# Kernel optimization log

Hardware: AMD Instinct MI355X
Metric: run time of the kernel (lower is better)

Reference implementation:

```python
import jax, jax.numpy as jnp
import numpy as np

B, N, D, H = 4, 1024, 1024, 16
DH = D // H
EPS = 1e-5


def setup_inputs() -> dict:
    key = jax.random.key(0)
    ks = jax.random.split(key, 16)
    s = lambda fan_in: 1.0 / np.sqrt(fan_in)
    inp = {
        'x0': jax.random.normal(ks[0], (B, N, D), jnp.float32),
        'x1': jax.random.normal(ks[1], (B, N, D), jnp.float32),
        # weights stored as [in, out]; y = x @ W + b
        'Wqk': jax.random.uniform(ks[2], (D, D), jnp.float32, -s(D), s(D)),
        'bqk': jax.random.uniform(ks[3], (D,), jnp.float32, -s(D), s(D)),
        'Wv': jax.random.uniform(ks[4], (D, D), jnp.float32, -s(D), s(D)),
        'bv': jax.random.uniform(ks[5], (D,), jnp.float32, -s(D), s(D)),
        'Wo': jax.random.uniform(ks[6], (D, D), jnp.float32, -s(D), s(D)),
        'bo': jax.random.uniform(ks[7], (D,), jnp.float32, -s(D), s(D)),
        'Wf1': jax.random.uniform(ks[8], (2 * D, 2 * D), jnp.float32, -s(2 * D), s(2 * D)),
        'bf1': jax.random.uniform(ks[9], (2 * D,), jnp.float32, -s(2 * D), s(2 * D)),
        'gamma': jnp.ones((2 * D,), jnp.float32),
        'beta': jnp.zeros((2 * D,), jnp.float32),
        'Wf2': jax.random.uniform(ks[10], (2 * D, D), jnp.float32, -s(2 * D), s(2 * D)),
        'bf2': jax.random.uniform(ks[11], (D,), jnp.float32, -s(2 * D), s(2 * D)),
    }
    return inp


def _heads(t):
    # [B, N, D] -> [B, H, N, DH]
    b, n, _ = t.shape
    return t.reshape(b, n, H, DH).transpose(0, 2, 1, 3)


def _merge(t):
    # [B, H, N, DH] -> [B, N, D]
    b, h, n, dh = t.shape
    return t.transpose(0, 2, 1, 3).reshape(b, n, h * dh)


def _ffn(z, Wf1, bf1, gamma, beta, Wf2, bf2):
    h = z @ Wf1 + bf1
    mu = jnp.mean(h, axis=-1, keepdims=True)
    var = jnp.mean((h - mu) ** 2, axis=-1, keepdims=True)
    h = (h - mu) * jax.lax.rsqrt(var + EPS) * gamma + beta
    h = jax.nn.gelu(h, approximate=False)
    return h @ Wf2 + bf2


def reference(x0, x1, Wqk, bqk, Wv, bv, Wo, bo, Wf1, bf1, gamma, beta, Wf2, bf2):
    scale = DH ** (-0.5)
    qk0 = _heads(x0 @ Wqk + bqk) * (scale ** 0.5)
    qk1 = _heads(x1 @ Wqk + bqk) * (scale ** 0.5)
    v0 = _heads(x0 @ Wv + bv)
    v1 = _heads(x1 @ Wv + bv)
    # shared similarity matrix [B, H, N0, N1]
    sim = jnp.einsum('bhid,bhjd->bhij', qk0, qk1)
    attn01 = jax.nn.softmax(sim, axis=-1)            # over N1
    attn10 = jax.nn.softmax(sim, axis=-2)            # over N0 (== softmax(sim^T, -1)^T)
    m0 = jnp.einsum('bhij,bhjd->bhid', attn01, v1)   # [B,H,N0,DH]
    m1 = jnp.einsum('bhji,bhjd->bhid', attn10, v0)   # [B,H,N1,DH]
    m0 = _merge(m0) @ Wo + bo
    m1 = _merge(m1) @ Wo + bo
    y0 = x0 + _ffn(jnp.concatenate([x0, m0], -1), Wf1, bf1, gamma, beta, Wf2, bf2)
    y1 = x1 + _ffn(jnp.concatenate([x1, m1], -1), Wf1, bf1, gamma, beta, Wf2, bf2)
    return (y0, y1)
```

## Files before the change

### kernel.cpp

```cpp
#include <hip/hip_runtime.h>
#include <hip/hip_bf16.h>

typedef unsigned short u16;
typedef unsigned int u32;
typedef __attribute__((ext_vector_type(8))) short bf16x8;
typedef __attribute__((ext_vector_type(4))) float f32x4;
typedef __attribute__((ext_vector_type(16))) float f32x16;

#define DEV __device__ __forceinline__
#define FENCE asm volatile("" ::: "memory")
#define WAITL asm volatile("s_waitcnt lgkmcnt(0)" ::: "memory")
#define BAR __builtin_amdgcn_s_barrier()
#define VMC(n) asm volatile("s_waitcnt vmcnt(" #n ")" ::: "memory")

static constexpr int Bc = 4, Nc = 1024, Dc = 1024, Hc = 16, Mc = 4096, D2c = 2048;
static constexpr size_t VT_STRIDE = (size_t)4 * 16 * 64 * 1024;

DEV u16 f2bf(float f) {
  u32 u = __builtin_bit_cast(u32, f);
  u = (u + 0x7FFFu + ((u >> 16) & 1u)) >> 16;
  return (u16)u;
}
DEV float bf2f(u16 h) { u32 u = ((u32)h) << 16; return __builtin_bit_cast(float, u); }
DEV void gl_lds16(const void* g, void* l) {
  __builtin_amdgcn_global_load_lds((const __attribute__((address_space(1))) u32*)g,
                                   (__attribute__((address_space(3))) u32*)l, 16, 0, 0);
}
DEV int SW(int r, int c) { return c ^ (r & 7) ^ ((r >> 3) & 3); }

DEV float erf_fast(float x) {
  float ax = __builtin_fabsf(x);
  float t = __builtin_amdgcn_rcpf(__builtin_fmaf(0.3275911f, ax, 1.0f));
  float p = __builtin_fmaf(1.061405429f, t, -1.453152027f);
  p = __builtin_fmaf(p, t, 1.421413741f);
  p = __builtin_fmaf(p, t, -0.284496736f);
  p = __builtin_fmaf(p, t, 0.254829592f);
  p *= t;
  float e = __builtin_amdgcn_exp2f(-1.4426950408889634f * ax * ax);
  float r = __builtin_fmaf(-p, e, 1.0f);
  return __builtin_copysignf(r, x);
}
DEV float gelu_exact(float v) {
  return 0.5f * v * (1.0f + erf_fast(v * 0.70710678118654752f));
}

__global__ __launch_bounds__(256) void k_f32_to_bf16(const float* __restrict__ in,
                                                     u16* __restrict__ out, int n) {
  int i = (blockIdx.x * 256 + threadIdx.x) * 8;
  if (i >= n) return;
  float4 a = *(const float4*)(in + i);
  float4 b = *(const float4*)(in + i + 4);
  union { u16 s[8]; uint4 v; } r;
  r.s[0] = f2bf(a.x); r.s[1] = f2bf(a.y); r.s[2] = f2bf(a.z); r.s[3] = f2bf(a.w);
  r.s[4] = f2bf(b.x); r.s[5] = f2bf(b.y); r.s[6] = f2bf(b.z); r.s[7] = f2bf(b.w);
  *(uint4*)(out + i) = r.v;
}

__global__ __launch_bounds__(256) void k_transpose_f32_bf16(const float* __restrict__ in,
                                                            u16* __restrict__ out, int R, int C) {
  __shared__ float t[64][65];
  int c0 = blockIdx.x * 64, r0 = blockIdx.y * 64;
  int tid = threadIdx.x;
  int rr = tid >> 4, cc4 = (tid & 15) * 4;
  for (int k = 0; k < 4; ++k) {
    int r = rr + k * 16;
    float4 v = *(const float4*)(in + (size_t)(r0 + r) * C + c0 + cc4);
    t[r][cc4 + 0] = v.x; t[r][cc4 + 1] = v.y; t[r][cc4 + 2] = v.z; t[r][cc4 + 3] = v.w;
  }
  __syncthreads();
  int cw = tid >> 4, rr4 = (tid & 15) * 4;
  for (int k = 0; k < 4; ++k) {
    int c = cw + k * 16;
    union { u16 s[4]; uint2 v; } p;
    for (int j = 0; j < 4; ++j) p.s[j] = f2bf(t[rr4 + j][c]);
    *(uint2*)(out + (size_t)(c0 + c) * R + r0 + rr4) = p.v;
  }
}

__global__ __launch_bounds__(256) void k_v_transpose(const u16* __restrict__ qkv,
                                                     u16* __restrict__ vt01) {
  __shared__ __align__(16) u16 t[64][80];
  int z = blockIdx.z;
  const u16* v = qkv + (size_t)z * Mc * 2048 + 1024;
  u16* vt = vt01 + (size_t)z * VT_STRIDE;
  int nt = blockIdx.x;
  int bh = blockIdx.y, b = bh >> 4, h = bh & 15;
  int tid = threadIdx.x;
  for (int it = 0; it < 2; ++it) {
    int u = it * 256 + tid; int r = u >> 3, ch = u & 7;
    uint4 raw = *(const uint4*)(v + ((size_t)b * Nc + nt * 64 + r) * 2048 + h * 64 + ch * 8);
    *(uint4*)&t[r][ch * 8] = raw;
  }
  __syncthreads();
  for (int it = 0; it < 2; ++it) {
    int u = it * 256 + tid; int d = u >> 3, nch = u & 7;
    union { u16 s[8]; uint4 v4; } p;
    for (int j = 0; j < 8; ++j) p.s[j] = t[nch * 8 + j][d];
    *(uint4*)(vt + ((size_t)bh * 64 + d) * Nc + nt * 64 + nch * 8) = p.v4;
  }
}

__global__ __launch_bounds__(512, 1) void k_gemm8(
    const u16* __restrict__ A1, int lda1, const u16* __restrict__ A2, int lda2, int kstile,
    const u16* __restrict__ Bt, const float* __restrict__ bias1, const float* __restrict__ bias2,
    int Nsplit, float scale1, float scale2, u16* __restrict__ out, int ldc, int K, int gx) {
  __shared__ __align__(16) u16 lds[65536];
  int tid = threadIdx.x;
  int w = tid >> 6, l = tid & 63;
  int lo = l & 15, hi = l >> 4;
  int wm2 = w >> 2, wn4 = w & 3;
  int nt = K >> 6, niter = nt >> 1;

  int nwg = gridDim.x;
  int swz = (blockIdx.x & 7) * (nwg >> 3) + (blockIdx.x >> 3);
  int m0 = (swz / gx) * 256, n0 = (swz % gx) * 256;

  auto ldsA = [&](int buf, int h) -> u16* { return lds + ((buf << 1) + h) * 8192; };
  auto ldsB = [&](int buf, int h) -> u16* { return lds + 32768 + ((buf << 1) + h) * 8192; };

  auto stageA = [&](int tile, int h) {
    int tt = tile < nt ? tile : 0;
    const u16* base; int ldx, kof;
    if (tt < kstile) { base = A1; ldx = lda1; kof = tt * 64; }
    else             { base = A2; ldx = lda2; kof = (tt - kstile) * 64; }
    u16* dst = ldsA(tile & 1, h);
    size_t row0 = (size_t)(m0 + h * 128);
#pragma unroll
    for (int i = 0; i < 2; ++i) {
      int e = i * 4096 + tid * 8;
      int r = e >> 6, s = (e >> 3) & 7;
      gl_lds16(base + (row0 + r) * (size_t)ldx + kof + 8 * (s ^ (r & 7)), dst + e);
    }
  };
  auto stageB = [&](int tile, int h) {
    int tt = tile < nt ? tile : 0;
    u16* dst = ldsB(tile & 1, h);
    size_t row0 = (size_t)(n0 + h * 128);
#pragma unroll
    for (int i = 0; i < 2; ++i) {
      int e = i * 4096 + tid * 8;
      int r = e >> 6, s = (e >> 3) & 7;
      gl_lds16(Bt + (row0 + r) * (size_t)K + tt * 64 + 8 * (s ^ (r & 7)), dst + e);
    }
  };
  auto loadA = [&](bf16x8 (&a)[4][2], int buf, int qm) {
    const u16* src = ldsA(buf, qm);
#pragma unroll
    for (int mf = 0; mf < 4; ++mf) {
      int r = wm2 * 64 + mf * 16 + lo;
#pragma unroll
      for (int kk = 0; kk < 2; ++kk)
        a[mf][kk] = *(const bf16x8*)&src[r * 64 + (((kk * 4 + hi) ^ (r & 7)) << 3)];
    }
  };
  auto loadB = [&](bf16x8 (&bq)[2][2], int buf, int qn) {
    const u16* src = ldsB(buf, qn);
#pragma unroll
    for (int nf = 0; nf < 2; ++nf) {
      int r = wn4 * 32 + nf * 16 + lo;
#pragma unroll
      for (int kk = 0; kk < 2; ++kk)
        bq[nf][kk] = *(const bf16x8*)&src[r * 64 + (((kk * 4 + hi) ^ (r & 7)) << 3)];
    }
  };

  f32x4 acc00[4][2] = {}, acc01[4][2] = {}, acc10[4][2] = {}, acc11[4][2] = {};
  bf16x8 a[4][2], b0[2][2], b1[2][2];

  auto mmaQ = [&](f32x4 (&accq)[4][2], bf16x8 (&aa)[4][2], bf16x8 (&bb)[2][2]) {
    __builtin_amdgcn_s_setprio(1);
#pragma unroll
    for (int mf = 0; mf < 4; ++mf)
#pragma unroll
      for (int nf = 0; nf < 2; ++nf)
#pragma unroll
        for (int kk = 0; kk < 2; ++kk)
          accq[mf][nf] = __builtin_amdgcn_mfma_f32_16x16x32_bf16(aa[mf][kk], bb[nf][kk], accq[mf][nf], 0, 0, 0);
    __builtin_amdgcn_s_setprio(0);
  };

  stageA(0, 0); stageB(0, 0); stageB(0, 1); stageA(0, 1);
  stageA(1, 0); stageB(1, 0); stageB(1, 1); stageA(1, 1);
  VMC(12); BAR;

  for (int it = 0; it < niter; ++it) {
    int t0 = 2 * it;
    loadA(a, 0, 0); loadB(b0, 0, 0);
    FENCE; BAR; WAITL;
    mmaQ(acc00, a, b0);
    FENCE; VMC(10); BAR;
    loadB(b1, 0, 1);
    stageA(t0 + 2, 0);
    FENCE; BAR; WAITL;
    mmaQ(acc01, a, b1);
    FENCE; VMC(10); BAR;
    loadA(a, 0, 1);
    stageB(t0 + 2, 0);
    FENCE; BAR; WAITL;
    mmaQ(acc10, a, b0);
    FENCE; BAR;
    stageB(t0 + 2, 1);
    FENCE; BAR;
    mmaQ(acc11, a, b1);
    FENCE; VMC(10); BAR;
    loadA(a, 1, 0); loadB(b0, 1, 0);
    stageA(t0 + 2, 1);
    FENCE; BAR; WAITL;
    mmaQ(acc00, a, b0);
    FENCE; VMC(10); BAR;
    loadB(b1, 1, 1);
    stageA(t0 + 3, 0);
    FENCE; BAR; WAITL;
    mmaQ(acc01, a, b1);
    FENCE; VMC(10); BAR;
    loadA(a, 1, 1);
    stageB(t0 + 3, 0);
    FENCE; BAR; WAITL;
    mmaQ(acc10, a, b0);
    FENCE; BAR;
    stageB(t0 + 3, 1); stageA(t0 + 3, 1);
    FENCE; BAR;
    mmaQ(acc11, a, b1);
    FENCE; VMC(12); BAR;
  }

  auto epi = [&](f32x4 (&accq)[4][2], int qm, int qn) {
#pragma unroll
    for (int mf = 0; mf < 4; ++mf)
#pragma unroll
      for (int nf = 0; nf < 2; ++nf) {
        int col = n0 + qn * 128 + wn4 * 32 + nf * 16 + lo;
        float bb, sc;
        if (col < Nsplit) { bb = bias1[col]; sc = scale1; }
        else              { bb = bias2[col - Nsplit]; sc = scale2; }
        int row = m0 + qm * 128 + wm2 * 64 + mf * 16 + hi * 4;
#pragma unroll
        for (int i = 0; i < 4; ++i)
          out[(size_t)(row + i) * ldc + col] = f2bf((accq[mf][nf][i] + bb) * sc);
      }
  };
  epi(acc00, 0, 0); epi(acc01, 0, 1); epi(acc10, 1, 0); epi(acc11, 1, 1);
}

template <bool OUT_BF16>
__global__ __launch_bounds__(512, 1) void k_gemm8h(
    const u16* __restrict__ A1, int lda1, const u16* __restrict__ Bt,
    const float* __restrict__ bias,
    const float* __restrict__ resid0, const float* __restrict__ resid1, int Msplit,
    void* __restrict__ out, int ldc, int K, int gx) {
  __shared__ __align__(16) u16 lds[49152];
  int tid = threadIdx.x;
  int w = tid >> 6, l = tid & 63;
  int lo = l & 15, hi = l >> 4;
  int wm2 = w >> 2, wn4 = w & 3;
  int nt = K >> 6, niter = nt >> 1;

  int nwg = gridDim.x;
  int swz = (blockIdx.x & 7) * (nwg >> 3) + (blockIdx.x >> 3);
  int m0 = (swz / gx) * 256, n0 = (swz % gx) * 128;

  auto ldsA = [&](int buf, int h) -> u16* { return lds + ((buf << 1) + h) * 8192; };
  auto ldsB = [&](int buf, int h) -> u16* { return lds + 32768 + ((buf << 1) + h) * 4096; };

  auto stageA = [&](int tile, int h) {
    int tt = tile < nt ? tile : 0;
    u16* dst = ldsA(tile & 1, h);
    size_t row0 = (size_t)(m0 + h * 128);
#pragma unroll
    for (int i = 0; i < 2; ++i) {
      int e = i * 4096 + tid * 8;
      int r = e >> 6, s = (e >> 3) & 7;
      gl_lds16(A1 + (row0 + r) * (size_t)lda1 + tt * 64 + 8 * (s ^ (r & 7)), dst + e);
    }
  };
  auto stageB = [&](int tile, int h) {
    int tt = tile < nt ? tile : 0;
    u16* dst = ldsB(tile & 1, h);
    size_t row0 = (size_t)(n0 + h * 64);
    int e = tid * 8;
    int r = e >> 6, s = (e >> 3) & 7;
    gl_lds16(Bt + (row0 + r) * (size_t)K + tt * 64 + 8 * (s ^ (r & 7)), dst + e);
  };
  auto loadA = [&](bf16x8 (&a)[4][2], int buf, int qm) {
    const u16* src = ldsA(buf, qm);
#pragma unroll
    for (int mf = 0; mf < 4; ++mf) {
      int r = wm2 * 64 + mf * 16 + lo;
#pragma unroll
      for (int kk = 0; kk < 2; ++kk)
        a[mf][kk] = *(const bf16x8*)&src[r * 64 + (((kk * 4 + hi) ^ (r & 7)) << 3)];
    }
  };
  auto loadB = [&](bf16x8 (&bq)[2], int buf, int qn) {
    const u16* src = ldsB(buf, qn);
    int r = wn4 * 16 + lo;
#pragma unroll
    for (int kk = 0; kk < 2; ++kk)
      bq[kk] = *(const bf16x8*)&src[r * 64 + (((kk * 4 + hi) ^ (r & 7)) << 3)];
  };

  f32x4 acc00[4] = {}, acc01[4] = {}, acc10[4] = {}, acc11[4] = {};
  bf16x8 a[4][2], b0[2], b1[2];

  auto mma8 = [&](f32x4 (&accq)[4], bf16x8 (&aa)[4][2], bf16x8 (&bb)[2]) {
    __builtin_amdgcn_s_setprio(1);
#pragma unroll
    for (int mf = 0; mf < 4; ++mf)
#pragma unroll
      for (int kk = 0; kk < 2; ++kk)
        accq[mf] = __builtin_amdgcn_mfma_f32_16x16x32_bf16(aa[mf][kk], bb[kk], accq[mf], 0, 0, 0);
    __builtin_amdgcn_s_setprio(0);
  };

  stageA(0, 0); stageB(0, 0); stageB(0, 1); stageA(0, 1);
  stageA(1, 0); stageB(1, 0); stageB(1, 1); stageA(1, 1);
  VMC(9); BAR;

  for (int it = 0; it < niter; ++it) {
    int t0 = 2 * it;
    loadA(a, 0, 0); loadB(b0, 0, 0);
    FENCE; BAR; WAITL;
    mma8(acc00, a, b0);
    FENCE; VMC(8); BAR;
    loadB(b1, 0, 1);
    stageA(t0 + 2, 0);
    FENCE; BAR; WAITL;
    mma8(acc01, a, b1);
    FENCE; VMC(8); BAR;
    loadA(a, 0, 1);
    stageB(t0 + 2, 0);
    FENCE; BAR; WAITL;
    mma8(acc10, a, b0);
    FENCE; BAR;
    stageB(t0 + 2, 1);
    FENCE; BAR;
    mma8(acc11, a, b1);
    FENCE; VMC(7); BAR;
    loadA(a, 1, 0); loadB(b0, 1, 0);
    stageA(t0 + 2, 1);
    FENCE; BAR; WAITL;
    mma8(acc00, a, b0);
    FENCE; VMC(8); BAR;
    loadB(b1, 1, 1);
    stageA(t0 + 3, 0);
    FENCE; BAR; WAITL;
    mma8(acc01, a, b1);
    FENCE; VMC(8); BAR;
    loadA(a, 1, 1);
    stageB(t0 + 3, 0);
    FENCE; BAR; WAITL;
    mma8(acc10, a, b0);
    FENCE; BAR;
    stageB(t0 + 3, 1); stageA(t0 + 3, 1);
    FENCE; BAR;
    mma8(acc11, a, b1);
    FENCE; VMC(9); BAR;
  }

  auto epi = [&](f32x4 (&accq)[4], int qm, int qn) {
    int col = n0 + qn * 64 + wn4 * 16 + lo;
    float bb = bias[col];
#pragma unroll
    for (int mf = 0; mf < 4; ++mf) {
      int row = m0 + qm * 128 + wm2 * 64 + mf * 16 + hi * 4;
      const float* rsd = nullptr; int roff = 0;
      if (resid0) { if (row < Msplit) { rsd = resid0; } else { rsd = resid1; roff = Msplit; } }
#pragma unroll
      for (int i = 0; i < 4; ++i) {
        float v = accq[mf][i] + bb;
        if (rsd) v += rsd[(size_t)(row + i - roff) * ldc + col];
        if (OUT_BF16) ((u16*)out)[(size_t)(row + i) * ldc + col] = f2bf(v);
        else          ((float*)out)[(size_t)(row + i) * ldc + col] = v;
      }
    }
  };
  epi(acc00, 0, 0); epi(acc01, 0, 1); epi(acc10, 1, 0); epi(acc11, 1, 1);
}

__global__ __launch_bounds__(512, 2) void k_attn(const u16* __restrict__ qkv,
                                                 const u16* __restrict__ vt01,
                                                 u16* __restrict__ m01) {
  __shared__ __align__(16) u16 q_lds[256 * 64];
  __shared__ __align__(16) u16 k_lds[2][64 * 64];
  __shared__ __align__(16) u16 v_lds[2][64 * 64];
  int z = blockIdx.z;
  const u16* Q  = qkv + (size_t)z * Mc * 2048;
  const u16* Kg = qkv + (size_t)(1 - z) * Mc * 2048;
  const u16* Vt = vt01 + (size_t)(1 - z) * VT_STRIDE;
  u16* Out = m01 + (size_t)z * Mc * Dc;
  int tid = threadIdx.x;
  int w = tid >> 6, l = tid & 63;
  int q31 = l & 31, h = l >> 5;
  int qt = blockIdx.x;
  int bh = blockIdx.y, b = bh >> 4, hd = bh & 15;
  size_t rowQ0 = (size_t)b * Nc + qt * 256;

  {
    int r = tid >> 3, s = tid & 7;
#pragma unroll
    for (int c = 0; c < 4; ++c)
      gl_lds16(Q + (rowQ0 + c * 64 + r) * 2048 + hd * 64 + 8 * SW(r, s),
               &q_lds[(size_t)(c * 512 + tid) * 8]);
    gl_lds16(Kg + ((size_t)b * Nc + r) * 2048 + hd * 64 + 8 * SW(r, s), &k_lds[0][(size_t)tid * 8]);
    gl_lds16(Vt + ((size_t)bh * 64 + r) * Nc + 8 * SW(r, s), &v_lds[0][(size_t)tid * 8]);
  }
  __syncthreads();

  bf16x8 qf[4];
  {
    int row = w * 32 + q31;
#pragma unroll
    for (int dk = 0; dk < 4; ++dk)
      qf[dk] = *(const bf16x8*)&q_lds[row * 64 + (SW(row, dk * 2 + h) << 3)];
  }

  f32x16 o0 = {}, o1 = {};
  float ls = 0.f;
  int cur = 0;

  for (int t = 0; t < Nc / 64; ++t) {
    if (t + 1 < Nc / 64) {
      int r = tid >> 3, s = tid & 7;
      gl_lds16(Kg + ((size_t)b * Nc + (t + 1) * 64 + r) * 2048 + hd * 64 + 8 * SW(r, s),
               &k_lds[cur ^ 1][(size_t)tid * 8]);
      gl_lds16(Vt + ((size_t)bh * 64 + r) * Nc + (t + 1) * 64 + 8 * SW(r, s),
               &v_lds[cur ^ 1][(size_t)tid * 8]);
    }

    f32x16 s0 = {}, s1 = {};
    __builtin_amdgcn_s_setprio(1);
#pragma unroll
    for (int dk = 0; dk < 4; ++dk) {
      int r0 = q31, r1 = 32 + q31;
      bf16x8 k0 = *(const bf16x8*)&k_lds[cur][r0 * 64 + (SW(r0, dk * 2 + h) << 3)];
      bf16x8 k1 = *(const bf16x8*)&k_lds[cur][r1 * 64 + (SW(r1, dk * 2 + h) << 3)];
      s0 = __builtin_amdgcn_mfma_f32_32x32x16_bf16(k0, qf[dk], s0, 0, 0, 0);
      s1 = __builtin_amdgcn_mfma_f32_32x32x16_bf16(k1, qf[dk], s1, 0, 0, 0);
    }
    __builtin_amdgcn_s_setprio(0);

    {
      float c16[16];
#pragma unroll
      for (int i = 0; i < 16; ++i) {
        float p0 = exp2f(s0[i]);
        float p1 = exp2f(s1[i]);
        s0[i] = p0; s1[i] = p1;
        c16[i] = p0 + p1;
      }
#pragma unroll
      for (int st = 8; st >= 1; st >>= 1)
#pragma unroll
        for (int i = 0; i < st; ++i) c16[i] += c16[i + st];
      u32 xa = __builtin_bit_cast(u32, c16[0]), xb = xa;
      asm("v_permlane32_swap_b32 %0, %1" : "+v"(xa), "+v"(xb));
      ls += __builtin_bit_cast(float, xa) + __builtin_bit_cast(float, xb);
    }

    u32 pk0[4][2], pk1[4][2];
#pragma unroll
    for (int a2 = 0; a2 < 4; ++a2)
#pragma unroll
      for (int c2 = 0; c2 < 2; ++c2) {
        asm("v_cvt_pk_bf16_f32 %0, %1, %2" : "=v"(pk0[a2][c2]) : "v"(s0[4 * a2 + 2 * c2]), "v"(s0[4 * a2 + 2 * c2 + 1]));
        asm("v_cvt_pk_bf16_f32 %0, %1, %2" : "=v"(pk1[a2][c2]) : "v"(s1[4 * a2 + 2 * c2]), "v"(s1[4 * a2 + 2 * c2 + 1]));
      }
    bf16x8 pf[4];
#pragma unroll
    for (int ks = 0; ks < 4; ++ks) {
      const int aE = (2 * ks) & 3, aO = (2 * ks + 1) & 3;
      u32 x0, y0, x1, y1;
      if (ks < 2) { x0 = pk0[aE][0]; y0 = pk0[aO][0]; x1 = pk0[aE][1]; y1 = pk0[aO][1]; }
      else        { x0 = pk1[aE][0]; y0 = pk1[aO][0]; x1 = pk1[aE][1]; y1 = pk1[aO][1]; }
      asm("v_permlane32_swap_b32 %0, %1" : "+v"(x0), "+v"(y0));
      asm("v_permlane32_swap_b32 %0, %1" : "+v"(x1), "+v"(y1));
      union { u32 u[4]; bf16x8 v; } fu;
      fu.u[0] = x0; fu.u[1] = x1; fu.u[2] = y0; fu.u[3] = y1;
      pf[ks] = fu.v;
    }

    __builtin_amdgcn_s_setprio(1);
#pragma unroll
    for (int ks = 0; ks < 4; ++ks) {
      int r0 = q31, r1 = 32 + q31;
      bf16x8 v0 = *(const bf16x8*)&v_lds[cur][r0 * 64 + (SW(r0, ks * 2 + h) << 3)];
      bf16x8 v1 = *(const bf16x8*)&v_lds[cur][r1 * 64 + (SW(r1, ks * 2 + h) << 3)];
      o0 = __builtin_amdgcn_mfma_f32_32x32x16_bf16(v0, pf[ks], o0, 0, 0, 0);
      o1 = __builtin_amdgcn_mfma_f32_32x32x16_bf16(v1, pf[ks], o1, 0, 0, 0);
    }
    __builtin_amdgcn_s_setprio(0);

    __syncthreads();
    cur ^= 1;
  }

  float inv = 1.f / ls;
  int q_abs = qt * 256 + w * 32 + q31;
  u16* orow = Out + ((size_t)b * Nc + q_abs) * Dc + hd * 64;
#pragma unroll
  for (int rq = 0; rq < 4; ++rq) {
    union { u16 s[4]; uint2 v; } p0, p1;
#pragma unroll
    for (int c = 0; c < 4; ++c) {
      p0.s[c] = f2bf(o0[4 * rq + c] * inv);
      p1.s[c] = f2bf(o1[4 * rq + c] * inv);
    }
    *(uint2*)(orow + 8 * rq + 4 * h) = p0.v;
    *(uint2*)(orow + 32 + 8 * rq + 4 * h) = p1.v;
  }
}

__global__ __launch_bounds__(256) void k_ln_gelu(u16* __restrict__ hbuf,
                                                 const float* __restrict__ gamma,
                                                 const float* __restrict__ beta) {
  int w = threadIdx.x >> 6, l = threadIdx.x & 63;
  int row = blockIdx.x * 4 + w;
  u16* hp = hbuf + (size_t)row * D2c;

  uint4 raw[4];
#pragma unroll
  for (int i = 0; i < 4; ++i)
    raw[i] = *(const uint4*)(hp + (i * 64 + l) * 8);

  float vals[32];
  float s = 0.f, s2 = 0.f;
#pragma unroll
  for (int i = 0; i < 4; ++i) {
    const u16* rs = (const u16*)&raw[i];
#pragma unroll
    for (int j = 0; j < 8; ++j) {
      float v = bf2f(rs[j]);
      vals[i * 8 + j] = v;
      s += v; s2 += v * v;
    }
  }
#pragma unroll
  for (int off = 1; off < 64; off <<= 1) {
    s += __shfl_xor(s, off);
    s2 += __shfl_xor(s2, off);
  }
  float mu = s * (1.f / D2c);
  float var = s2 * (1.f / D2c) - mu * mu;
  float rstd = rsqrtf(var + 1e-5f);

#pragma unroll
  for (int i = 0; i < 4; ++i) {
    int cbase = (i * 64 + l) * 8;
    float4 g0 = *(const float4*)(gamma + cbase);
    float4 g1 = *(const float4*)(gamma + cbase + 4);
    float4 b0 = *(const float4*)(beta + cbase);
    float4 b1 = *(const float4*)(beta + cbase + 4);
    float g[8] = {g0.x, g0.y, g0.z, g0.w, g1.x, g1.y, g1.z, g1.w};
    float bt[8] = {b0.x, b0.y, b0.z, b0.w, b1.x, b1.y, b1.z, b1.w};
    union { u16 s[8]; uint4 v; } o;
#pragma unroll
    for (int j = 0; j < 8; ++j) {
      float v = (vals[i * 8 + j] - mu) * rstd * g[j] + bt[j];
      o.s[j] = f2bf(gelu_exact(v));
    }
    *(uint4*)(hp + cbase) = o.v;
  }
}

extern "C" void kernel_launch(void* const* d_in, const int* in_sizes, int n_in,
                              void* d_out, int out_size, void* d_ws, size_t ws_size,
                              hipStream_t stream) {
  const float* x0   = (const float*)d_in[0];
  const float* x1   = (const float*)d_in[1];
  const float* Wqk  = (const float*)d_in[2];
  const float* bqk  = (const float*)d_in[3];
  const float* Wv   = (const float*)d_in[4];
  const float* bv   = (const float*)d_in[5];
  const float* Wo   = (const float*)d_in[6];
  const float* bo   = (const float*)d_in[7];
  const float* Wf1  = (const float*)d_in[8];
  const float* bf1  = (const float*)d_in[9];
  const float* gamma= (const float*)d_in[10];
  const float* beta = (const float*)d_in[11];
  const float* Wf2  = (const float*)d_in[12];
  const float* bf2  = (const float*)d_in[13];
  float* y = (float*)d_out;

  char* p = (char*)d_ws;
  auto take = [&](size_t elems) { u16* r = (u16*)p; p += ((elems * 2 + 255) & ~(size_t)255); return r; };
  u16* Wqkvt = take((size_t)2048 * 1024);
  u16* Wot   = take((size_t)1024 * 1024);
  u16* Wf1t  = take((size_t)2048 * 2048);
  u16* Wf2t  = take((size_t)2048 * 1024);
  u16* x01b  = take((size_t)8192 * 1024);
  u16* qkv   = take((size_t)8192 * 2048);
  u16* vt01  = take(2 * VT_STRIDE);
  u16* m01   = take((size_t)8192 * 1024);
  u16* h01 = qkv;
  u16* o01 = vt01;

  dim3 blk(256);
  const float sq = 0.4246608984f;

  k_transpose_f32_bf16<<<dim3(16, 16), blk, 0, stream>>>(Wqk, Wqkvt, 1024, 1024);
  k_transpose_f32_bf16<<<dim3(16, 16), blk, 0, stream>>>(Wv, Wqkvt + (size_t)1024 * 1024, 1024, 1024);
  k_transpose_f32_bf16<<<dim3(16, 16), blk, 0, stream>>>(Wo, Wot, 1024, 1024);
  k_transpose_f32_bf16<<<dim3(32, 32), blk, 0, stream>>>(Wf1, Wf1t, 2048, 2048);
  k_transpose_f32_bf16<<<dim3(16, 32), blk, 0, stream>>>(Wf2, Wf2t, 2048, 1024);
  k_f32_to_bf16<<<dim3(2048), blk, 0, stream>>>(x0, x01b, 4096 * 1024);
  k_f32_to_bf16<<<dim3(2048), blk, 0, stream>>>(x1, x01b + (size_t)4096 * 1024, 4096 * 1024);

  k_gemm8<<<dim3(256), dim3(512), 0, stream>>>(
      x01b, 1024, x01b, 1024, 16, Wqkvt,
      bqk, bv, 1024, sq, 1.f, qkv, 2048, 1024, 8);

  k_v_transpose<<<dim3(16, 64, 2), blk, 0, stream>>>(qkv, vt01);

  k_attn<<<dim3(4, 64, 2), dim3(512), 0, stream>>>(qkv, vt01, m01);

  k_gemm8h<true><<<dim3(256), dim3(512), 0, stream>>>(
      m01, 1024, Wot, bo, nullptr, nullptr, 0, o01, 1024, 1024, 8);

  k_gemm8<<<dim3(256), dim3(512), 0, stream>>>(
      x01b, 1024, o01, 1024, 16, Wf1t,
      bf1, nullptr, 2048, 1.f, 1.f, h01, 2048, 2048, 8);

  k_ln_gelu<<<dim3(2048), blk, 0, stream>>>(h01, gamma, beta);

  k_gemm8h<false><<<dim3(256), dim3(512), 0, stream>>>(
      h01, 2048, Wf2t, bf2, x0, x1, 4096, y, 1024, 2048, 8);
}
```

Measured before the change: 285.2 us.

## Double-buffer A fragments and overlap LDS reads with MFMA in GEMM main loops

```diff
diff --git a/kernel.cpp b/kernel.cpp
--- a/kernel.cpp
+++ b/kernel.cpp
@@ -9,9 +9,10 @@
 
 #define DEV __device__ __forceinline__
 #define FENCE asm volatile("" ::: "memory")
-#define WAITL asm volatile("s_waitcnt lgkmcnt(0)" ::: "memory")
 #define BAR __builtin_amdgcn_s_barrier()
 #define VMC(n) asm volatile("s_waitcnt vmcnt(" #n ")" ::: "memory")
+#define LGKM(n) asm volatile("s_waitcnt lgkmcnt(" #n ")" ::: "memory")
+#define SGB __builtin_amdgcn_sched_barrier(0)
 
 static constexpr int Bc = 4, Nc = 1024, Dc = 1024, Hc = 16, Mc = 4096, D2c = 2048;
 static constexpr size_t VT_STRIDE = (size_t)4 * 16 * 64 * 1024;
@@ -165,63 +166,68 @@
   };
 
   f32x4 acc00[4][2] = {}, acc01[4][2] = {}, acc10[4][2] = {}, acc11[4][2] = {};
-  bf16x8 a[4][2], b0[2][2], b1[2][2];
+  bf16x8 a_A[4][2], a_B[4][2], b0[2][2], b1[2][2];
 
   auto mmaQ = [&](f32x4 (&accq)[4][2], bf16x8 (&aa)[4][2], bf16x8 (&bb)[2][2]) {
     __builtin_amdgcn_s_setprio(1);
 #pragma unroll
-    for (int mf = 0; mf < 4; ++mf)
-#pragma unroll
-      for (int nf = 0; nf < 2; ++nf)
-#pragma unroll
-        for (int kk = 0; kk < 2; ++kk)
+    for (int kk = 0; kk < 2; ++kk)
+#pragma unroll
+      for (int mf = 0; mf < 4; ++mf)
+#pragma unroll
+        for (int nf = 0; nf < 2; ++nf)
           accq[mf][nf] = __builtin_amdgcn_mfma_f32_16x16x32_bf16(aa[mf][kk], bb[nf][kk], accq[mf][nf], 0, 0, 0);
     __builtin_amdgcn_s_setprio(0);
   };
 
   stageA(0, 0); stageB(0, 0); stageB(0, 1); stageA(0, 1);
   stageA(1, 0); stageB(1, 0); stageB(1, 1); stageA(1, 1);
-  VMC(12); BAR;
+  VMC(10); BAR;
+  loadA(a_A, 0, 0);
+  loadB(b0, 0, 0);
+  FENCE;
 
   for (int it = 0; it < niter; ++it) {
     int t0 = 2 * it;
-    loadA(a, 0, 0); loadB(b0, 0, 0);
-    FENCE; BAR; WAITL;
-    mmaQ(acc00, a, b0);
-    FENCE; VMC(10); BAR;
     loadB(b1, 0, 1);
+    LGKM(4); SGB;
+    mmaQ(acc00, a_A, b0);
+    VMC(8); BAR;
+    loadA(a_B, 0, 1);
     stageA(t0 + 2, 0);
-    FENCE; BAR; WAITL;
-    mmaQ(acc01, a, b1);
-    FENCE; VMC(10); BAR;
-    loadA(a, 0, 1);
+    LGKM(8); SGB;
+    mmaQ(acc01, a_A, b1);
+    BAR;
     stageB(t0 + 2, 0);
-    FENCE; BAR; WAITL;
-    mmaQ(acc10, a, b0);
-    FENCE; BAR;
+    LGKM(0); SGB;
+    mmaQ(acc11, a_B, b1);
+    VMC(8); BAR;
+    loadA(a_A, 1, 0);
     stageB(t0 + 2, 1);
-    FENCE; BAR;
-    mmaQ(acc11, a, b1);
-    FENCE; VMC(10); BAR;
-    loadA(a, 1, 0); loadB(b0, 1, 0);
+    SGB;
+    mmaQ(acc10, a_B, b0);
+    loadB(b0, 1, 0);
+    VMC(6); BAR;
+    loadB(b1, 1, 1);
     stageA(t0 + 2, 1);
-    FENCE; BAR; WAITL;
-    mmaQ(acc00, a, b0);
-    FENCE; VMC(10); BAR;
-    loadB(b1, 1, 1);
+    LGKM(4); SGB;
+    mmaQ(acc00, a_A, b0);
+    BAR;
+    loadA(a_B, 1, 1);
     stageA(t0 + 3, 0);
-    FENCE; BAR; WAITL;
-    mmaQ(acc01, a, b1);
-    FENCE; VMC(10); BAR;
-    loadA(a, 1, 1);
+    LGKM(8); SGB;
+    mmaQ(acc01, a_A, b1);
+    BAR;
     stageB(t0 + 3, 0);
-    FENCE; BAR; WAITL;
-    mmaQ(acc10, a, b0);
-    FENCE; BAR;
+    LGKM(0); SGB;
+    mmaQ(acc11, a_B, b1);
+    VMC(8); BAR;
+    loadA(a_A, 0, 0);
     stageB(t0 + 3, 1); stageA(t0 + 3, 1);
-    FENCE; BAR;
-    mmaQ(acc11, a, b1);
-    FENCE; VMC(12); BAR;
+    SGB;
+    mmaQ(acc10, a_B, b0);
+    loadB(b0, 0, 0);
+    VMC(10); BAR;
   }
 
   auto epi = [&](f32x4 (&accq)[4][2], int qm, int qn) {
@@ -239,7 +245,7 @@
           out[(size_t)(row + i) * ldc + col] = f2bf((accq[mf][nf][i] + bb) * sc);
       }
   };
-  epi(acc00, 0, 0); epi(acc01, 0, 1); epi(acc10, 1, 0); epi(acc11, 1, 1);
+  epi(acc00, 0, 0); epi(acc01, 0, 1); epi(acc11, 1, 1); epi(acc10, 1, 0);
 }
 
 template <bool OUT_BF16>
@@ -300,61 +306,66 @@
   };
 
   f32x4 acc00[4] = {}, acc01[4] = {}, acc10[4] = {}, acc11[4] = {};
-  bf16x8 a[4][2], b0[2], b1[2];
+  bf16x8 a_A[4][2], a_B[4][2], b0[2], b1[2];
 
   auto mma8 = [&](f32x4 (&accq)[4], bf16x8 (&aa)[4][2], bf16x8 (&bb)[2]) {
     __builtin_amdgcn_s_setprio(1);
 #pragma unroll
-    for (int mf = 0; mf < 4; ++mf)
-#pragma unroll
-      for (int kk = 0; kk < 2; ++kk)
+    for (int kk = 0; kk < 2; ++kk)
+#pragma unroll
+      for (int mf = 0; mf < 4; ++mf)
         accq[mf] = __builtin_amdgcn_mfma_f32_16x16x32_bf16(aa[mf][kk], bb[kk], accq[mf], 0, 0, 0);
     __builtin_amdgcn_s_setprio(0);
   };
 
   stageA(0, 0); stageB(0, 0); stageB(0, 1); stageA(0, 1);
   stageA(1, 0); stageB(1, 0); stageB(1, 1); stageA(1, 1);
-  VMC(9); BAR;
+  VMC(8); BAR;
+  loadA(a_A, 0, 0);
+  loadB(b0, 0, 0);
+  FENCE;
 
   for (int it = 0; it < niter; ++it) {
     int t0 = 2 * it;
-    loadA(a, 0, 0); loadB(b0, 0, 0);
-    FENCE; BAR; WAITL;
-    mma8(acc00, a, b0);
-    FENCE; VMC(8); BAR;
     loadB(b1, 0, 1);
+    LGKM(2); SGB;
+    mma8(acc00, a_A, b0);
+    VMC(6); BAR;
+    loadA(a_B, 0, 1);
     stageA(t0 + 2, 0);
-    FENCE; BAR; WAITL;
-    mma8(acc01, a, b1);
-    FENCE; VMC(8); BAR;
-    loadA(a, 0, 1);
+    LGKM(8); SGB;
+    mma8(acc01, a_A, b1);
+    BAR;
     stageB(t0 + 2, 0);
-    FENCE; BAR; WAITL;
-    mma8(acc10, a, b0);
-    FENCE; BAR;
+    LGKM(0); SGB;
+    mma8(acc11, a_B, b1);
+    VMC(6); BAR;
+    loadA(a_A, 1, 0);
     stageB(t0 + 2, 1);
-    FENCE; BAR;
-    mma8(acc11, a, b1);
-    FENCE; VMC(7); BAR;
-    loadA(a, 1, 0); loadB(b0, 1, 0);
+    SGB;
+    mma8(acc10, a_B, b0);
+    loadB(b0, 1, 0);
+    VMC(4); BAR;
+    loadB(b1, 1, 1);
     stageA(t0 + 2, 1);
-    FENCE; BAR; WAITL;
-    mma8(acc00, a, b0);
-    FENCE; VMC(8); BAR;
-    loadB(b1, 1, 1);
+    LGKM(2); SGB;
+    mma8(acc00, a_A, b0);
+    BAR;
+    loadA(a_B, 1, 1);
     stageA(t0 + 3, 0);
-    FENCE; BAR; WAITL;
-    mma8(acc01, a, b1);
-    FENCE; VMC(8); BAR;
-    loadA(a, 1, 1);
+    LGKM(8); SGB;
+    mma8(acc01, a_A, b1);
+    BAR;
     stageB(t0 + 3, 0);
-    FENCE; BAR; WAITL;
-    mma8(acc10, a, b0);
-    FENCE; BAR;
+    LGKM(0); SGB;
+    mma8(acc11, a_B, b1);
+    VMC(6); BAR;
+    loadA(a_A, 0, 0);
     stageB(t0 + 3, 1); stageA(t0 + 3, 1);
-    FENCE; BAR;
-    mma8(acc11, a, b1);
-    FENCE; VMC(9); BAR;
+    SGB;
+    mma8(acc10, a_B, b0);
+    loadB(b0, 0, 0);
+    VMC(8); BAR;
   }
 
   auto epi = [&](f32x4 (&accq)[4], int qm, int qn) {
@@ -374,7 +385,7 @@
       }
     }
   };
-  epi(acc00, 0, 0); epi(acc01, 0, 1); epi(acc10, 1, 0); epi(acc11, 1, 1);
+  epi(acc00, 0, 0); epi(acc01, 0, 1); epi(acc11, 1, 1); epi(acc10, 1, 0);
 }
 
 __global__ __launch_bounds__(512, 2) void k_attn(const u16* __restrict__ qkv,
```

Measured after the change: 346.7 us. 21.6% more time.
